# Performance work log

Hardware: AMD Instinct MI355X
Metric: run time of the kernel (lower is better)

Reference implementation:

```python
import jax, jax.numpy as jnp
import numpy as np
from jax import lax

IN_CH = 256
UP = 8
DN = ('NCHW', 'OIHW', 'NCHW')


def setup_inputs() -> dict:
    key = jax.random.key(0)
    ks = jax.random.split(key, 6)
    B, H, W = 8, 96, 96
    flow_lr = jax.random.normal(ks[0], (B, 2, H, W), dtype=jnp.float32)
    feat = jax.random.normal(ks[1], (B, IN_CH, H, W), dtype=jnp.float32)
    w1 = jax.random.normal(ks[2], (IN_CH, IN_CH, 3, 3), dtype=jnp.float32) * 0.02
    b1 = jnp.zeros((IN_CH,), dtype=jnp.float32)
    w2 = jax.random.normal(ks[3], (UP * UP * 9, IN_CH, 1, 1), dtype=jnp.float32) * 0.02
    b2 = jnp.zeros((UP * UP * 9,), dtype=jnp.float32)
    return {"flow_lr": flow_lr, "feat": feat, "w1": w1, "b1": b1, "w2": w2, "b2": b2}


def reference(flow_lr, feat, w1, b1, w2, b2):
    B, _, H, W = flow_lr.shape
    up = UP
    # mask head: 3x3 conv + relu + 1x1 conv
    x = lax.conv_general_dilated(feat, w1, (1, 1), 'SAME', dimension_numbers=DN)
    x = jax.nn.relu(x + b1[None, :, None, None])
    mask = lax.conv_general_dilated(x, w2, (1, 1), 'SAME', dimension_numbers=DN)
    mask = mask + b2[None, :, None, None]
    # channel dim 9*up*up splits as (9, up, up), matching torch .view(B,1,9,up,up,H,W)
    mask = mask.reshape(B, 9, up, up, H, W)
    mask = jax.nn.softmax(mask, axis=1)
    # unfold(flow_lr, 3, padding=1): 9 zero-padded 3x3 shifts, row-major (kh, kw)
    pad = jnp.pad(flow_lr, ((0, 0), (0, 0), (1, 1), (1, 1)))
    flow_unf = jnp.stack(
        [pad[:, :, i:i + H, j:j + W] for i in range(3) for j in range(3)], axis=2
    )  # (B, 2, 9, H, W)
    # convex combination over the 9 neighbors
    up_flow = jnp.einsum('bkpqhw,bckhw->bcpqhw', mask, flow_unf)  # (B,2,up,up,H,W)
    # pixel-shuffle: (B,2,p,q,H,W) -> (B,2,H,p,W,q) -> (B,2,H*up,W*up)
    up_flow = up_flow.transpose(0, 1, 4, 2, 5, 3).reshape(B, 2, H * up, W * up)
    return up_flow * up
```

## Files before the change

### kernel.cpp

```cpp
#include <hip/hip_runtime.h>
#include <hip/hip_bf16.h>
#include <stdint.h>

typedef unsigned short u16;
typedef __bf16 bf16x8 __attribute__((ext_vector_type(8)));
typedef float f32x4 __attribute__((ext_vector_type(4)));

#define MFMA16(a, b, c) __builtin_amdgcn_mfma_f32_16x16x32_bf16((a), (b), (c), 0, 0, 0)

#define GLOAD16(g, l)                                                        \
  __builtin_amdgcn_global_load_lds(                                          \
      (const __attribute__((address_space(1))) void*)(g),                    \
      (__attribute__((address_space(3))) void*)(l), 16, 0, 0)

static __device__ __forceinline__ u16 f2bf(float f) {
  union { float f; uint32_t u; } v;
  v.f = f;
  uint32_t u = v.u;
  return (u16)((u + 0x7FFFu + ((u >> 16) & 1u)) >> 16);
}

#define FEATT_ELEMS (8u * 98u * 98u * 256u)
#define W1T_OFF     FEATT_ELEMS
#define W1T_ELEMS   (256u * 2304u)
#define W2B_OFF     (W1T_OFF + W1T_ELEMS)

__global__ __launch_bounds__(256) void halo_zero(u16* __restrict__ featT) {
  int tid = blockIdx.x * 256 + threadIdx.x;
  int b = tid / (388 * 32);
  int rem = tid % (388 * 32);
  int pos = rem >> 5, v = rem & 31;
  int h, w;
  if (pos < 98) { h = 0; w = pos; }
  else if (pos < 196) { h = 97; w = pos - 98; }
  else if (pos < 292) { h = pos - 196 + 1; w = 0; }
  else { h = pos - 292 + 1; w = 97; }
  uint4* dst = (uint4*)(featT + (size_t)((b * 98 + h) * 98 + w) * 256 + v * 8);
  *dst = make_uint4(0, 0, 0, 0);
}

__global__ __launch_bounds__(256) void prep_featT(const float* __restrict__ feat,
                                                  u16* __restrict__ featT) {
  const int pt = blockIdx.x, ct = blockIdx.y, b = blockIdx.z;
  const int p0 = pt * 64, c0 = ct * 64;
  __shared__ float tile[64][65];
  const int t = threadIdx.x;
  const int pj = t & 63, ci0 = t >> 6;
#pragma unroll
  for (int r = 0; r < 16; ++r) {
    int ci = r * 4 + ci0;
    tile[ci][pj] = feat[(b * 256 + c0 + ci) * 9216 + p0 + pj];
  }
  __syncthreads();
  const int pl = t >> 2, cc0 = (t & 3) * 16;
  const int pix = p0 + pl;
  const int h = pix / 96, w = pix % 96;
  uint32_t u[8];
#pragma unroll
  for (int i = 0; i < 8; ++i) {
    u16 lo = f2bf(tile[cc0 + 2 * i][pl]);
    u16 hi = f2bf(tile[cc0 + 2 * i + 1][pl]);
    u[i] = (uint32_t)lo | ((uint32_t)hi << 16);
  }
  uint4* dst = (uint4*)(featT + (size_t)((b * 98 + h + 1) * 98 + (w + 1)) * 256 + c0 + cc0);
  dst[0] = make_uint4(u[0], u[1], u[2], u[3]);
  dst[1] = make_uint4(u[4], u[5], u[6], u[7]);
}

__global__ __launch_bounds__(256) void prep_w(const float* __restrict__ w1,
                                              const float* __restrict__ w2,
                                              u16* __restrict__ w1t,
                                              u16* __restrict__ w2b) {
  int i = blockIdx.x * 256 + threadIdx.x;
  if (i < 589824) {
    int oc = i / 2304, r = i % 2304;
    int tap = r >> 8, cin = r & 255;
    w1t[i] = f2bf(w1[(oc * 256 + cin) * 9 + tap]);
  } else {
    int j = i - 589824;
    if (j < 147456) w2b[j] = f2bf(w2[j]);
  }
}

__global__ __launch_bounds__(512, 2) void fused(const u16* __restrict__ featT,
                                                const u16* __restrict__ w1t,
                                                const float* __restrict__ b1,
                                                const u16* __restrict__ w2b,
                                                const float* __restrict__ b2,
                                                const float* __restrict__ flow,
                                                float* __restrict__ out) {
  __shared__ __align__(16) u16 smem[61440];
  __shared__ float sFlow[2][9][96];
  __shared__ float sb1[256];
  __shared__ float sb2[576];

  const int t = threadIdx.x;
  const int wave = t >> 6, lane = t & 63;
  const int bid = blockIdx.x;
  const int mt = (bid & 7) * 96 + (bid >> 3);
  const int b = mt / 96;
  const int h0 = mt % 96;

  if (t < 256) sb1[t] = b1[t];
  for (int i = t; i < 576; i += 512) sb2[i] = b2[i];
  for (int i = t; i < 1728; i += 512) {
    int c = i / 864, rem = i % 864;
    int k = rem / 96, p = rem % 96;
    int hh = h0 + k / 3 - 1, ww = p + k % 3 - 1;
    float v = 0.f;
    if (hh >= 0 && hh < 96 && ww >= 0 && ww < 96)
      v = flow[((b * 2 + c) * 96 + hh) * 96 + ww];
    sFlow[c][k][p] = v;
  }

  const u16* aBase[2];
#pragma unroll
  for (int r = 0; r < 2; ++r) {
    int row = (r * 8 + wave) * 8 + (lane >> 3);
    int chunk = (lane & 7) ^ (row & 7);
    aBase[r] = featT + ((size_t)(b * 98 + h0 + 1) * 98 + (row + 1)) * 256 + chunk * 8;
  }
  const u16* bBase[4];
#pragma unroll
  for (int r = 0; r < 4; ++r) {
    int row = (r * 8 + wave) * 8 + (lane >> 3);
    int chunk = (lane & 7) ^ (row & 7);
    bBase[r] = w1t + (size_t)row * 2304 + chunk * 8;
  }

  auto stageA = [&](int kt, int bufi) {
    int tap = kt >> 2;
    int dh = tap / 3 - 1, dw = tap % 3 - 1;
    int aoff = (dh * 98 + dw) * 256 + (kt & 3) * 64;
    int boff = kt * 64;
    u16* base = &smem[bufi * 22528];
#pragma unroll
    for (int r = 0; r < 2; ++r) {
      int wr = r * 8 + wave;
      if (wr < 12) GLOAD16(aBase[r] + aoff, base + wr * 512);
    }
#pragma unroll
    for (int r = 0; r < 4; ++r)
      GLOAD16(bBase[r] + boff, base + 6144 + (r * 8 + wave) * 512);
  };

  const int wm = wave >> 2, wn = wave & 3;
  int aoffs[3][2], boffs[4][2];
#pragma unroll
  for (int ki = 0; ki < 2; ++ki) {
    int kc = ki * 4 + (lane >> 4);
#pragma unroll
    for (int m = 0; m < 3; ++m) {
      int rowa = wm * 48 + m * 16 + (lane & 15);
      aoffs[m][ki] = rowa * 64 + ((kc ^ (rowa & 7)) * 8);
    }
#pragma unroll
    for (int n = 0; n < 4; ++n) {
      int rowb = wn * 64 + n * 16 + (lane & 15);
      boffs[n][ki] = rowb * 64 + ((kc ^ (rowb & 7)) * 8);
    }
  }

  f32x4 acc[3][4];
#pragma unroll
  for (int m = 0; m < 3; ++m)
#pragma unroll
    for (int n = 0; n < 4; ++n) acc[m][n] = f32x4{0.f, 0.f, 0.f, 0.f};

  stageA(0, 0);
  __syncthreads();
  int buf = 0;
  for (int kt = 0; kt < 36; ++kt) {
    if (kt < 35) stageA(kt + 1, buf ^ 1);
    const u16* base = &smem[buf * 22528];
#pragma unroll
    for (int ki = 0; ki < 2; ++ki) {
      bf16x8 av[3], bv[4];
#pragma unroll
      for (int m = 0; m < 3; ++m) av[m] = *(const bf16x8*)&base[aoffs[m][ki]];
#pragma unroll
      for (int n = 0; n < 4; ++n) bv[n] = *(const bf16x8*)&base[6144 + boffs[n][ki]];
#pragma unroll
      for (int m = 0; m < 3; ++m)
#pragma unroll
        for (int n = 0; n < 4; ++n) acc[m][n] = MFMA16(av[m], bv[n], acc[m][n]);
    }
    __syncthreads();
    buf ^= 1;
  }

  const int g4 = (lane >> 4) << 2;
#pragma unroll
  for (int m = 0; m < 3; ++m) {
    int pixr = wm * 48 + m * 16 + g4;
#pragma unroll
    for (int n = 0; n < 4; ++n) {
      int oc = wn * 64 + n * 16 + (lane & 15);
      float bias = sb1[oc];
      f32x4 v = acc[m][n];
#pragma unroll
      for (int j = 0; j < 4; ++j) {
        int pix = pixr + j;
        float val = v[j] + bias;
        val = val > 0.f ? val : 0.f;
        smem[pix * 256 + (((oc >> 3) ^ (pix & 7)) * 8) + (oc & 7)] = f2bf(val);
      }
    }
  }
  __syncthreads();

  auto stageB = [&](int step, int bufi) {
    int cI = step >> 1, kh = step & 1;
    u16* base = &smem[24576 + bufi * 18432];
#pragma unroll
    for (int r = 0; r < 5; ++r) {
      int wr = r * 8 + wave;
      if (wr < 36) {
        int row = wr * 4 + (lane >> 4);
        int chan = (row >> 4) * 64 + cI * 16 + (row & 15);
        int c = lane & 15;
        const u16* src = w2b + (size_t)chan * 256 + kh * 128 + ((c ^ (row & 15)) * 8);
        GLOAD16(src, base + wr * 512);
      }
    }
  };

  stageB(0, 0);
  bf16x8 areg[8];
  const int pixl = wave * 16 + (lane & 15);
  if (wave < 6) {
#pragma unroll
    for (int s = 0; s < 8; ++s) {
      int kc = s * 4 + (lane >> 4);
      areg[s] = *(const bf16x8*)&smem[pixl * 256 + ((kc ^ (pixl & 7)) * 8)];
    }
  }
  __syncthreads();

  f32x4 acc2[9];
  int bufc = 0;
#pragma unroll
  for (int step = 0; step < 8; ++step) {
    if (step < 7) stageB(step + 1, bufc ^ 1);
    const int kh = step & 1, cI = step >> 1;
    if (wave < 6) {
      if (kh == 0) {
#pragma unroll
        for (int nf = 0; nf < 9; ++nf) acc2[nf] = f32x4{0.f, 0.f, 0.f, 0.f};
      }
      const u16* base = &smem[24576 + bufc * 18432];
#pragma unroll
      for (int ki = 0; ki < 4; ++ki) {
        bf16x8 a = areg[kh * 4 + ki];
        int kc = ki * 4 + (lane >> 4);
#pragma unroll
        for (int nf = 0; nf < 9; ++nf) {
          int row = nf * 16 + (lane & 15);
          bf16x8 bv = *(const bf16x8*)&base[row * 128 + ((kc ^ (row & 15)) * 8)];
          acc2[nf] = MFMA16(a, bv, acc2[nf]);
        }
      }
      if (kh == 1) {
        int pql = lane & 15;
        int p = cI * 2 + (pql >> 3), q = pql & 7;
#pragma unroll
        for (int j = 0; j < 4; ++j) {
          int pe = wave * 16 + g4 + j;
          float v[9], mx = -3.0e38f;
#pragma unroll
          for (int nf = 0; nf < 9; ++nf) {
            v[nf] = acc2[nf][j] + sb2[nf * 64 + cI * 16 + pql];
            mx = fmaxf(mx, v[nf]);
          }
          float s = 0.f, fx = 0.f, fy = 0.f;
#pragma unroll
          for (int nf = 0; nf < 9; ++nf) {
            float e = __expf(v[nf] - mx);
            s += e;
            fx += e * sFlow[0][nf][pe];
            fy += e * sFlow[1][nf][pe];
          }
          float sc = 8.0f / s;
          size_t o0 = ((size_t)(b * 2 + 0) * 768 + h0 * 8 + p) * 768 + pe * 8 + q;
          size_t o1 = ((size_t)(b * 2 + 1) * 768 + h0 * 8 + p) * 768 + pe * 8 + q;
          out[o0] = fx * sc;
          out[o1] = fy * sc;
        }
      }
    }
    __syncthreads();
    bufc ^= 1;
  }
}

extern "C" void kernel_launch(void* const* d_in, const int* in_sizes, int n_in,
                              void* d_out, int out_size, void* d_ws, size_t ws_size,
                              hipStream_t stream) {
  const float* flow = (const float*)d_in[0];
  const float* feat = (const float*)d_in[1];
  const float* w1 = (const float*)d_in[2];
  const float* b1 = (const float*)d_in[3];
  const float* w2 = (const float*)d_in[4];
  const float* b2 = (const float*)d_in[5];
  float* out = (float*)d_out;
  u16* ws = (u16*)d_ws;
  u16* featT = ws;
  u16* w1t = ws + W1T_OFF;
  u16* w2b = ws + W2B_OFF;

  halo_zero<<<388, 256, 0, stream>>>(featT);
  prep_featT<<<dim3(144, 4, 8), 256, 0, stream>>>(feat, featT);
  prep_w<<<2880, 256, 0, stream>>>(w1, w2, w1t, w2b);
  fused<<<768, 512, 0, stream>>>(featT, w1t, b1, w2b, b2, flow, out);
}
```

Measured before the change: 202.0 us.

## Prefetch two stages ahead with explicit vmcnt waits and raised MFMA priority

Restructures both GEMM loops (3x3 conv and 1x1 mask conv) so two async global-to-LDS stages are in flight at once. __syncthreads is replaced with targeted s_waitcnt vmcnt/lgkmcnt plus raw s_barrier and sched_barrier, so a wave waits only on the older load group. MFMA sections are wrapped in s_setprio(1) to favour matrix issue across waves. This aims to hide global load latency, but it relies on hand-counted vmcnt values matching the number of loads each stage issues.

```diff
diff --git a/kernel.cpp b/kernel.cpp
--- a/kernel.cpp
+++ b/kernel.cpp
@@ -12,6 +12,9 @@
   __builtin_amdgcn_global_load_lds(                                          \
       (const __attribute__((address_space(1))) void*)(g),                    \
       (__attribute__((address_space(3))) void*)(l), 16, 0, 0)
+
+#define SBAR() __builtin_amdgcn_s_barrier()
+#define SCHEDBAR() __builtin_amdgcn_sched_barrier(0)
 
 static __device__ __forceinline__ u16 f2bf(float f) {
   union { float f; uint32_t u; } v;
@@ -167,12 +170,9 @@
 #pragma unroll
     for (int n = 0; n < 4; ++n) acc[m][n] = f32x4{0.f, 0.f, 0.f, 0.f};
 
-  stageA(0, 0);
-  __syncthreads();
-  int buf = 0;
-  for (int kt = 0; kt < 36; ++kt) {
-    if (kt < 35) stageA(kt + 1, buf ^ 1);
-    const u16* base = &smem[buf * 22528];
+  auto computeA = [&](int bufi) {
+    const u16* base = &smem[bufi * 22528];
+    __builtin_amdgcn_s_setprio(1);
 #pragma unroll
     for (int ki = 0; ki < 2; ++ki) {
       bf16x8 av[3], bv[4];
@@ -185,9 +185,32 @@
 #pragma unroll
         for (int n = 0; n < 4; ++n) acc[m][n] = MFMA16(av[m], bv[n], acc[m][n]);
     }
-    __syncthreads();
-    buf ^= 1;
-  }
+    __builtin_amdgcn_s_setprio(0);
+  };
+
+  __syncthreads();
+  stageA(0, 0);
+  stageA(1, 1);
+
+  for (int kt = 0; kt < 34; ++kt) {
+    asm volatile("s_waitcnt vmcnt(5)" ::: "memory");
+    SBAR();
+    SCHEDBAR();
+    computeA(kt & 1);
+    asm volatile("s_waitcnt lgkmcnt(0)" ::: "memory");
+    SBAR();
+    SCHEDBAR();
+    stageA(kt + 2, kt & 1);
+  }
+  asm volatile("s_waitcnt vmcnt(5)" ::: "memory");
+  SBAR(); SCHEDBAR();
+  computeA(0);
+  asm volatile("s_waitcnt lgkmcnt(0)" ::: "memory");
+  SBAR(); SCHEDBAR();
+  asm volatile("s_waitcnt vmcnt(0)" ::: "memory");
+  SBAR(); SCHEDBAR();
+  computeA(1);
+  __syncthreads();
 
   const int g4 = (lane >> 4) << 2;
 #pragma unroll
@@ -226,6 +249,7 @@
   };
 
   stageB(0, 0);
+  stageB(1, 1);
   bf16x8 areg[8];
   const int pixl = wave * 16 + (lane & 15);
   if (wave < 6) {
@@ -235,20 +259,23 @@
       areg[s] = *(const bf16x8*)&smem[pixl * 256 + ((kc ^ (pixl & 7)) * 8)];
     }
   }
-  __syncthreads();
 
   f32x4 acc2[9];
-  int bufc = 0;
 #pragma unroll
   for (int step = 0; step < 8; ++step) {
-    if (step < 7) stageB(step + 1, bufc ^ 1);
+    if (step == 7) asm volatile("s_waitcnt vmcnt(0)" ::: "memory");
+    else           asm volatile("s_waitcnt vmcnt(4)" ::: "memory");
+    SBAR();
+    SCHEDBAR();
     const int kh = step & 1, cI = step >> 1;
+    const int bufc = step & 1;
     if (wave < 6) {
       if (kh == 0) {
 #pragma unroll
         for (int nf = 0; nf < 9; ++nf) acc2[nf] = f32x4{0.f, 0.f, 0.f, 0.f};
       }
       const u16* base = &smem[24576 + bufc * 18432];
+      __builtin_amdgcn_s_setprio(1);
 #pragma unroll
       for (int ki = 0; ki < 4; ++ki) {
         bf16x8 a = areg[kh * 4 + ki];
@@ -260,6 +287,7 @@
           acc2[nf] = MFMA16(a, bv, acc2[nf]);
         }
       }
+      __builtin_amdgcn_s_setprio(0);
       if (kh == 1) {
         int pql = lane & 15;
         int p = cI * 2 + (pql >> 3), q = pql & 7;
@@ -288,8 +316,10 @@
         }
       }
     }
-    __syncthreads();
-    bufc ^= 1;
+    asm volatile("s_waitcnt lgkmcnt(0)" ::: "memory");
+    SBAR();
+    SCHEDBAR();
+    if (step < 6) stageB(step + 2, step & 1);
   }
 }
 
```

Measured after the change: 205.8 us. No clear change (+1.9%).
